# Optimization experiments

Measured on AMD Instinct MI355X. Metric: run time of the kernel, lower is better.

## Reference

```python
import jax, jax.numpy as jnp
import numpy as np

B, LVS, WIDTH, DEPTH = 8192, 512, 512, 7
EPS = 1e-5
SLOPE = 0.01  # torch LeakyReLU default negative_slope


def setup_inputs() -> dict:
    key = jax.random.key(0)
    ks = jax.random.split(key, 16)
    inp = {"x": jax.random.normal(ks[0], (B, LVS), dtype=jnp.float32)}
    for i in range(DEPTH):
        fan_in = LVS + WIDTH * i
        inp[f"W{i}"] = jax.random.normal(ks[1 + i], (WIDTH, fan_in), dtype=jnp.float32) / np.sqrt(fan_in)
    inp["b"] = 0.01 * jax.random.normal(ks[8], (DEPTH, WIDTH), dtype=jnp.float32)
    inp["gamma"] = jnp.ones((DEPTH, WIDTH), dtype=jnp.float32)
    inp["beta"] = jnp.zeros((DEPTH, WIDTH), dtype=jnp.float32)
    cin = LVS + DEPTH * WIDTH  # 4096
    inp["Wc"] = jax.random.normal(ks[9], (1, cin), dtype=jnp.float32) / np.sqrt(cin)
    inp["bc"] = jnp.zeros((1,), dtype=jnp.float32)
    # torch: rv = randn(...) * 0.02 + 1, multiplied onto each projection
    inp["noise"] = 1.0 + 0.02 * jax.random.normal(ks[10], (DEPTH, B, WIDTH), dtype=jnp.float32)
    return inp


def reference(x, W0, W1, W2, W3, W4, W5, W6, b, gamma, beta, Wc, bc, noise):
    Ws = (W0, W1, W2, W3, W4, W5, W6)
    last = x
    for i in range(DEPTH):
        # Linear: [B, in_i] @ [in_i, width]
        h = jnp.einsum('bi,wi->bw', last, Ws[i]) + b[i]
        # BatchNorm1d (training mode: batch stats, biased variance)
        mean = jnp.mean(h, axis=0)
        var = jnp.mean(jnp.square(h - mean), axis=0)
        h = (h - mean) * jax.lax.rsqrt(var + EPS) * gamma[i] + beta[i]
        # LeakyReLU + multiplicative noise, fused elementwise
        h = jnp.where(h >= 0, h, SLOPE * h) * noise[i]
        last = jnp.concatenate((last, h), axis=-1)
    logits = jnp.einsum('bi,oi->bo', last, Wc) + bc
    return jax.nn.sigmoid(logits)
```

## Files before the change

### kernel.cpp

```cpp
#include <hip/hip_runtime.h>

#define B_ROWS 8192
#define WIDTH  512
#define DEPTH  7
#define CIN    4096
#define EPS    1e-5f
#define SLOPE  0.01f

typedef __attribute__((ext_vector_type(8))) short short8;
typedef __attribute__((ext_vector_type(4))) short short4v;
typedef __attribute__((ext_vector_type(4))) float f32x4;
typedef __attribute__((ext_vector_type(16))) float f32x16;

__device__ inline short f2bf(float f) {
  unsigned u = __builtin_bit_cast(unsigned, f);
  unsigned r = (u + 0x7FFFu + ((u >> 16) & 1u)) >> 16;
  return (short)r;
}

__device__ inline float bf2f(short b) {
  unsigned u = ((unsigned)(unsigned short)b) << 16;
  return __builtin_bit_cast(float, u);
}

__device__ inline void gl_lds16(const void* g, void* l) {
  __builtin_amdgcn_global_load_lds(
      (const __attribute__((address_space(1))) unsigned*)g,
      (__attribute__((address_space(3))) unsigned*)l, 16, 0, 0);
}

struct WP { const float* p[7]; };

__global__ __launch_bounds__(256) void prolog(WP wp, short* __restrict__ wbf,
                                              const float* __restrict__ x,
                                              const float* __restrict__ wc,
                                              short* __restrict__ lastbf,
                                              float* __restrict__ logit,
                                              float* __restrict__ sumsz) {
  if (blockIdx.x >= 2048) {
    long e = ((long)(blockIdx.x - 2048) * 256 + threadIdx.x) * 8;
    int layer; long base;
    if      (e < 262144L)  { layer = 0; base = 0; }
    else if (e < 786432L)  { layer = 1; base = 262144L; }
    else if (e < 1572864L) { layer = 2; base = 786432L; }
    else if (e < 2621440L) { layer = 3; base = 1572864L; }
    else if (e < 3932160L) { layer = 4; base = 2621440L; }
    else if (e < 5505024L) { layer = 5; base = 3932160L; }
    else                   { layer = 6; base = 5505024L; }
    const float* src = wp.p[layer] + (e - base);
    f32x4 v0 = *(const f32x4*)src;
    f32x4 v1 = *(const f32x4*)(src + 4);
    short8 o;
    o[0] = f2bf(v0.x); o[1] = f2bf(v0.y); o[2] = f2bf(v0.z); o[3] = f2bf(v0.w);
    o[4] = f2bf(v1.x); o[5] = f2bf(v1.y); o[6] = f2bf(v1.z); o[7] = f2bf(v1.w);
    *(short8*)(wbf + e) = o;
    return;
  }
  int gid = blockIdx.x * 256 + threadIdx.x;
  if (gid < DEPTH * 1024) sumsz[gid] = 0.f;
  int w = threadIdx.x >> 6, l = threadIdx.x & 63;
  int r = blockIdx.x * 4 + w;
  const float* xr = x + (long)r * 512 + l * 8;
  f32x4 v0 = *(const f32x4*)xr;
  f32x4 v1 = *(const f32x4*)(xr + 4);
  const float* wcr = wc + l * 8;
  float acc = 0.f;
  short8 ob;
#pragma unroll
  for (int j = 0; j < 4; ++j) { acc += v0[j] * wcr[j];     ob[j]     = f2bf(v0[j]); }
#pragma unroll
  for (int j = 0; j < 4; ++j) { acc += v1[j] * wcr[4 + j]; ob[4 + j] = f2bf(v1[j]); }
  *(short8*)&lastbf[(long)r * CIN + l * 8] = ob;
#pragma unroll
  for (int off = 32; off; off >>= 1) acc += __shfl_xor(acc, off);
  if (l == 0) logit[r] = acc;
}

__global__ __launch_bounds__(256, 2) void gemm_fused(const short* __restrict__ A,
                                                     const short* __restrict__ Bw,
                                                     short* __restrict__ C,
                                                     float* __restrict__ sums,
                                                     int K) {
  __shared__ __align__(16) char smem[49152];
  int t = threadIdx.x;
  int ks = t >> 6, l = t & 63;
  int l31 = l & 31, hi = l >> 5;
  int bm = blockIdx.x, bn = blockIdx.y;
  const short* Ab = A + (long)(bm * 128) * CIN;
  const short* Bb = Bw + (long)(bn * 64) * K;

  f32x16 acc[4][2];
#pragma unroll
  for (int m = 0; m < 4; ++m)
#pragma unroll
    for (int n = 0; n < 2; ++n)
#pragma unroll
      for (int r = 0; r < 16; ++r) acc[m][n][r] = 0.f;

  int l8 = l >> 3;
  int scol = ((l & 7) ^ l8) << 3;

#define STAGE(buf, k0)                                                                       \
  {                                                                                          \
    char* base = smem + (buf) * 24576;                                                       \
    int c0 = ks * 4, c1 = ks * 2;                                                            \
    gl_lds16(Ab + (long)((c0    ) * 8 + l8) * CIN + (k0) + scol, base + (c0    ) * 1024);    \
    gl_lds16(Ab + (long)((c0 + 1) * 8 + l8) * CIN + (k0) + scol, base + (c0 + 1) * 1024);    \
    gl_lds16(Ab + (long)((c0 + 2) * 8 + l8) * CIN + (k0) + scol, base + (c0 + 2) * 1024);    \
    gl_lds16(Ab + (long)((c0 + 3) * 8 + l8) * CIN + (k0) + scol, base + (c0 + 3) * 1024);    \
    gl_lds16(Bb + (long)((c1    ) * 8 + l8) * K + (k0) + scol, base + 16384 + (c1    ) * 1024); \
    gl_lds16(Bb + (long)((c1 + 1) * 8 + l8) * K + (k0) + scol, base + 16384 + (c1 + 1) * 1024); \
  }

  STAGE(0, 0);
  __syncthreads();

  int kb = ks * 32 + hi * 16;
  int sw = (l & 7) << 4;

  int nt = K >> 6;
  int cur = 0;
  for (int tix = 0; tix < nt; ++tix) {
    if (tix + 1 < nt) STAGE(cur ^ 1, (tix + 1) << 6);
    const char* AsC = smem + cur * 24576;
    const char* BsC = AsC + 16384;
    short8 a[4], b[2];
#pragma unroll
    for (int m = 0; m < 4; ++m)
      a[m] = *(const short8*)(AsC + (m * 32 + l31) * 128 + (kb ^ sw));
#pragma unroll
    for (int n = 0; n < 2; ++n)
      b[n] = *(const short8*)(BsC + (n * 32 + l31) * 128 + (kb ^ sw));
#pragma unroll
    for (int m = 0; m < 4; ++m)
#pragma unroll
      for (int n = 0; n < 2; ++n)
        acc[m][n] = __builtin_amdgcn_mfma_f32_32x32x16_bf16(a[m], b[n], acc[m][n], 0, 0, 0);
    __syncthreads();
    cur ^= 1;
  }

  float* Red = (float*)smem;
#define RIDX(m, n, r) (((m) * 32 + ((r) & 3) + 8 * ((r) >> 2) + 4 * hi) * 64 + (n) * 32 + l31)
  if (ks == 3) {
#pragma unroll
    for (int m = 0; m < 4; ++m)
#pragma unroll
      for (int n = 0; n < 2; ++n)
#pragma unroll
        for (int r = 0; r < 16; ++r) Red[RIDX(m, n, r)] = acc[m][n][r];
  }
  __syncthreads();
  if (ks == 2) {
#pragma unroll
    for (int m = 0; m < 4; ++m)
#pragma unroll
      for (int n = 0; n < 2; ++n)
#pragma unroll
        for (int r = 0; r < 16; ++r) Red[RIDX(m, n, r)] += acc[m][n][r];
  }
  __syncthreads();
  if (ks == 1) {
#pragma unroll
    for (int m = 0; m < 4; ++m)
#pragma unroll
      for (int n = 0; n < 2; ++n)
#pragma unroll
        for (int r = 0; r < 16; ++r) Red[RIDX(m, n, r)] += acc[m][n][r];
  }
  __syncthreads();
  if (ks == 0) {
    short* Cb = C + (long)(bm * 128) * WIDTH + bn * 64;
#pragma unroll
    for (int n = 0; n < 2; ++n) {
      float s = 0.f, q = 0.f;
#pragma unroll
      for (int m = 0; m < 4; ++m) {
#pragma unroll
        for (int r = 0; r < 16; ++r) {
          int cr = (r & 3) + 8 * (r >> 2) + 4 * hi;
          float v = acc[m][n][r] + Red[RIDX(m, n, r)];
          Cb[(long)(m * 32 + cr) * WIDTH + n * 32 + l31] = f2bf(v);
          s += v; q += v * v;
        }
      }
      s += __shfl_xor(s, 32);
      q += __shfl_xor(q, 32);
      if (l < 32) {
        int colg = bn * 64 + n * 32 + l;
        atomicAdd(&sums[colg], s);
        atomicAdd(&sums[WIDTH + colg], q);
      }
    }
  }
#undef RIDX
#undef STAGE
}

__global__ __launch_bounds__(256) void bnact(const short* __restrict__ h,
                                             const float* __restrict__ sums,
                                             const float* __restrict__ gamma,
                                             const float* __restrict__ beta,
                                             const float* __restrict__ noise,
                                             const float* __restrict__ wc,
                                             short* __restrict__ lastseg,
                                             float* __restrict__ logit) {
  int w = threadIdx.x >> 6, l = threadIdx.x & 63;
  int r = blockIdx.x * 4 + w;
  int c = l * 8;
  const float invB = 1.0f / 8192.0f;
  short8 hb = *(const short8*)&h[(long)r * WIDTH + c];
  f32x4 n0 = *(const f32x4*)&noise[(long)r * WIDTH + c];
  f32x4 n1 = *(const f32x4*)&noise[(long)r * WIDTH + c + 4];
  float acc = 0.f;
  short8 ob;
#pragma unroll
  for (int j = 0; j < 8; ++j) {
    int cc = c + j;
    float hv = bf2f(hb[j]);
    float nv = j < 4 ? n0[j] : n1[j - 4];
    float mean = sums[cc] * invB;
    float var = sums[WIDTH + cc] * invB - mean * mean;
    float v = (hv - mean) * rsqrtf(var + EPS);
    v = v * gamma[cc] + beta[cc];
    v = v >= 0.f ? v : SLOPE * v;
    v *= nv;
    acc += v * wc[cc];
    ob[j] = f2bf(v);
  }
  *(short8*)&lastseg[(long)r * CIN + c] = ob;
#pragma unroll
  for (int off = 32; off; off >>= 1) acc += __shfl_xor(acc, off);
  if (l == 0) logit[r] += acc;
}

__global__ __launch_bounds__(256) void bnact_last(const short* __restrict__ h,
                                                  const float* __restrict__ sums,
                                                  const float* __restrict__ gamma,
                                                  const float* __restrict__ beta,
                                                  const float* __restrict__ noise,
                                                  const float* __restrict__ wc,
                                                  const float* __restrict__ logit,
                                                  const float* __restrict__ bc,
                                                  float* __restrict__ out) {
  int w = threadIdx.x >> 6, l = threadIdx.x & 63;
  int r = blockIdx.x * 4 + w;
  int c = l * 8;
  const float invB = 1.0f / 8192.0f;
  short8 hb = *(const short8*)&h[(long)r * WIDTH + c];
  f32x4 n0 = *(const f32x4*)&noise[(long)r * WIDTH + c];
  f32x4 n1 = *(const f32x4*)&noise[(long)r * WIDTH + c + 4];
  float acc = 0.f;
#pragma unroll
  for (int j = 0; j < 8; ++j) {
    int cc = c + j;
    float hv = bf2f(hb[j]);
    float nv = j < 4 ? n0[j] : n1[j - 4];
    float mean = sums[cc] * invB;
    float var = sums[WIDTH + cc] * invB - mean * mean;
    float v = (hv - mean) * rsqrtf(var + EPS);
    v = v * gamma[cc] + beta[cc];
    v = v >= 0.f ? v : SLOPE * v;
    v *= nv;
    acc += v * wc[cc];
  }
#pragma unroll
  for (int off = 32; off; off >>= 1) acc += __shfl_xor(acc, off);
  if (l == 0) {
    float z = logit[r] + acc + bc[0];
    out[r] = 1.0f / (1.0f + expf(-z));
  }
}

extern "C" void kernel_launch(void* const* d_in, const int* in_sizes, int n_in,
                              void* d_out, int out_size, void* d_ws, size_t ws_size,
                              hipStream_t stream) {
  (void)in_sizes; (void)n_in; (void)out_size; (void)ws_size;
  const float* x     = (const float*)d_in[0];
  WP wp;
  for (int i = 0; i < 7; ++i) wp.p[i] = (const float*)d_in[1 + i];
  const float* gamma = (const float*)d_in[9];
  const float* beta  = (const float*)d_in[10];
  const float* Wc    = (const float*)d_in[11];
  const float* bc    = (const float*)d_in[12];
  const float* noise = (const float*)d_in[13];

  char* ws = (char*)d_ws;
  short* lastbf = (short*)ws;
  short* hpre   = (short*)(ws + 67108864);
  short* wbf    = (short*)(ws + 67108864 + 16777216);
  float* sums   = (float*)(ws + 67108864 + 16777216 + 14680064);
  float* logit  = (float*)(ws + 67108864 + 16777216 + 14680064 + 28672);

  prolog<<<5632, 256, 0, stream>>>(wp, wbf, x, Wc, lastbf, logit, sums);

  long woff = 0;
  for (int i = 0; i < DEPTH; ++i) {
    int K = 512 * (i + 1);
    gemm_fused<<<dim3(64, 8), 256, 0, stream>>>(lastbf, wbf + woff, hpre,
                                                sums + i * 1024, K);
    if (i < DEPTH - 1) {
      bnact<<<2048, 256, 0, stream>>>(hpre, sums + i * 1024,
                                      gamma + i * 512, beta + i * 512,
                                      noise + (long)i * B_ROWS * WIDTH,
                                      Wc + 512 + i * 512,
                                      lastbf + 512 + (long)i * 512, logit);
    } else {
      bnact_last<<<2048, 256, 0, stream>>>(hpre, sums + i * 1024,
                                           gamma + i * 512, beta + i * 512,
                                           noise + (long)i * B_ROWS * WIDTH,
                                           Wc + 512 + i * 512,
                                           logit, bc, (float*)d_out);
    }
    woff += (long)512 * K;
  }
}
```

Baseline: 271.8 us.

## Pre-pack weights in MFMA fragment layout and load B directly to registers

The prolog now writes the bf16 weights in a k-blocked layout, grouped 8 k-values per column, so each lane's MFMA B fragment is one contiguous 16-byte global load. The GEMM stops staging B through LDS, loads B fragments straight into registers one tile ahead, and cuts the LDS buffer to A only. This saves LDS traffic and space, which may allow more occupancy. The cost is direct global loads with latency exposed in registers and extra register pressure.

```diff
diff --git a/kernel.cpp b/kernel.cpp
--- a/kernel.cpp
+++ b/kernel.cpp
@@ -30,6 +30,20 @@
 }
 
 struct WP { const float* p[7]; };
+
+template <int L>
+__device__ inline void convw_one(const float* __restrict__ src,
+                                 short* __restrict__ dst, int idx) {
+  constexpr int FAN = 512 * (L + 1);
+  int col = idx / FAN;
+  int k = idx - col * FAN;
+  f32x4 v0 = *(const f32x4*)(src + idx);
+  f32x4 v1 = *(const f32x4*)(src + idx + 4);
+  short8 o;
+  o[0] = f2bf(v0.x); o[1] = f2bf(v0.y); o[2] = f2bf(v0.z); o[3] = f2bf(v0.w);
+  o[4] = f2bf(v1.x); o[5] = f2bf(v1.y); o[6] = f2bf(v1.z); o[7] = f2bf(v1.w);
+  *(short8*)(dst + ((long)(k >> 3) << 12) + (col << 3)) = o;
+}
 
 __global__ __launch_bounds__(256) void prolog(WP wp, short* __restrict__ wbf,
                                               const float* __restrict__ x,
@@ -38,22 +52,14 @@
                                               float* __restrict__ logit,
                                               float* __restrict__ sumsz) {
   if (blockIdx.x >= 2048) {
-    long e = ((long)(blockIdx.x - 2048) * 256 + threadIdx.x) * 8;
-    int layer; long base;
-    if      (e < 262144L)  { layer = 0; base = 0; }
-    else if (e < 786432L)  { layer = 1; base = 262144L; }
-    else if (e < 1572864L) { layer = 2; base = 786432L; }
-    else if (e < 2621440L) { layer = 3; base = 1572864L; }
-    else if (e < 3932160L) { layer = 4; base = 2621440L; }
-    else if (e < 5505024L) { layer = 5; base = 3932160L; }
-    else                   { layer = 6; base = 5505024L; }
-    const float* src = wp.p[layer] + (e - base);
-    f32x4 v0 = *(const f32x4*)src;
-    f32x4 v1 = *(const f32x4*)(src + 4);
-    short8 o;
-    o[0] = f2bf(v0.x); o[1] = f2bf(v0.y); o[2] = f2bf(v0.z); o[3] = f2bf(v0.w);
-    o[4] = f2bf(v1.x); o[5] = f2bf(v1.y); o[6] = f2bf(v1.z); o[7] = f2bf(v1.w);
-    *(short8*)(wbf + e) = o;
+    int e = (int)(((long)(blockIdx.x - 2048) * 256 + threadIdx.x) * 8);
+    if      (e < 262144)  convw_one<0>(wp.p[0], wbf,           e);
+    else if (e < 786432)  convw_one<1>(wp.p[1], wbf + 262144,  e - 262144);
+    else if (e < 1572864) convw_one<2>(wp.p[2], wbf + 786432,  e - 786432);
+    else if (e < 2621440) convw_one<3>(wp.p[3], wbf + 1572864, e - 1572864);
+    else if (e < 3932160) convw_one<4>(wp.p[4], wbf + 2621440, e - 2621440);
+    else if (e < 5505024) convw_one<5>(wp.p[5], wbf + 3932160, e - 3932160);
+    else                  convw_one<6>(wp.p[6], wbf + 5505024, e - 5505024);
     return;
   }
   int gid = blockIdx.x * 256 + threadIdx.x;
@@ -81,13 +87,12 @@
                                                      short* __restrict__ C,
                                                      float* __restrict__ sums,
                                                      int K) {
-  __shared__ __align__(16) char smem[49152];
+  __shared__ __align__(16) char smem[32768];
   int t = threadIdx.x;
   int ks = t >> 6, l = t & 63;
   int l31 = l & 31, hi = l >> 5;
   int bm = blockIdx.x, bn = blockIdx.y;
   const short* Ab = A + (long)(bm * 128) * CIN;
-  const short* Bb = Bw + (long)(bn * 64) * K;
 
   f32x16 acc[4][2];
 #pragma unroll
@@ -100,18 +105,26 @@
   int l8 = l >> 3;
   int scol = ((l & 7) ^ l8) << 3;
 
-#define STAGE(buf, k0)                                                                       \
-  {                                                                                          \
-    char* base = smem + (buf) * 24576;                                                       \
-    int c0 = ks * 4, c1 = ks * 2;                                                            \
-    gl_lds16(Ab + (long)((c0    ) * 8 + l8) * CIN + (k0) + scol, base + (c0    ) * 1024);    \
-    gl_lds16(Ab + (long)((c0 + 1) * 8 + l8) * CIN + (k0) + scol, base + (c0 + 1) * 1024);    \
-    gl_lds16(Ab + (long)((c0 + 2) * 8 + l8) * CIN + (k0) + scol, base + (c0 + 2) * 1024);    \
-    gl_lds16(Ab + (long)((c0 + 3) * 8 + l8) * CIN + (k0) + scol, base + (c0 + 3) * 1024);    \
-    gl_lds16(Bb + (long)((c1    ) * 8 + l8) * K + (k0) + scol, base + 16384 + (c1    ) * 1024); \
-    gl_lds16(Bb + (long)((c1 + 1) * 8 + l8) * K + (k0) + scol, base + 16384 + (c1 + 1) * 1024); \
-  }
-
+#define STAGE(buf, k0)                                                                     \
+  {                                                                                        \
+    char* base = smem + (buf) * 16384;                                                     \
+    int c0 = ks * 4;                                                                       \
+    gl_lds16(Ab + (long)((c0    ) * 8 + l8) * CIN + (k0) + scol, base + (c0    ) * 1024);  \
+    gl_lds16(Ab + (long)((c0 + 1) * 8 + l8) * CIN + (k0) + scol, base + (c0 + 1) * 1024);  \
+    gl_lds16(Ab + (long)((c0 + 2) * 8 + l8) * CIN + (k0) + scol, base + (c0 + 2) * 1024);  \
+    gl_lds16(Ab + (long)((c0 + 3) * 8 + l8) * CIN + (k0) + scol, base + (c0 + 3) * 1024);  \
+  }
+
+  const short* Bp = Bw + ((ks * 2 + hi) << 12) + ((bn * 64 + l31) << 3);
+#define BLOAD(d0, d1, tt)                          \
+  {                                                \
+    const short* bp_ = Bp + ((long)(tt) << 15);    \
+    d0 = *(const short8*)bp_;                      \
+    d1 = *(const short8*)(bp_ + 256);              \
+  }
+
+  short8 bc0, bc1, bn0, bn1;
+  BLOAD(bc0, bc1, 0);
   STAGE(0, 0);
   __syncthreads();
 
@@ -121,23 +134,23 @@
   int nt = K >> 6;
   int cur = 0;
   for (int tix = 0; tix < nt; ++tix) {
-    if (tix + 1 < nt) STAGE(cur ^ 1, (tix + 1) << 6);
-    const char* AsC = smem + cur * 24576;
-    const char* BsC = AsC + 16384;
-    short8 a[4], b[2];
+    if (tix + 1 < nt) {
+      STAGE(cur ^ 1, (tix + 1) << 6);
+      BLOAD(bn0, bn1, tix + 1);
+    }
+    const char* AsC = smem + cur * 16384;
+    short8 a[4];
 #pragma unroll
     for (int m = 0; m < 4; ++m)
       a[m] = *(const short8*)(AsC + (m * 32 + l31) * 128 + (kb ^ sw));
 #pragma unroll
-    for (int n = 0; n < 2; ++n)
-      b[n] = *(const short8*)(BsC + (n * 32 + l31) * 128 + (kb ^ sw));
-#pragma unroll
-    for (int m = 0; m < 4; ++m)
-#pragma unroll
-      for (int n = 0; n < 2; ++n)
-        acc[m][n] = __builtin_amdgcn_mfma_f32_32x32x16_bf16(a[m], b[n], acc[m][n], 0, 0, 0);
+    for (int m = 0; m < 4; ++m) {
+      acc[m][0] = __builtin_amdgcn_mfma_f32_32x32x16_bf16(a[m], bc0, acc[m][0], 0, 0, 0);
+      acc[m][1] = __builtin_amdgcn_mfma_f32_32x32x16_bf16(a[m], bc1, acc[m][1], 0, 0, 0);
+    }
     __syncthreads();
     cur ^= 1;
+    bc0 = bn0; bc1 = bn1;
   }
 
   float* Red = (float*)smem;
@@ -194,6 +207,7 @@
     }
   }
 #undef RIDX
+#undef BLOAD
 #undef STAGE
 }
 
```

Result: slower. 296.1 us (+9.0%).
